# Performance work log

Hardware: AMD Instinct MI355X
Metric: run time of the kernel (lower is better)

Reference implementation:

```python
import jax, jax.numpy as jnp
import numpy as np

N_NODES = 100000


def gcn_conv(x, W, b, src, dst, n):
    """PyG GCNConv with default add_self_loops and symmetric normalization."""
    xw = x @ W  # [N, out]
    loop = jnp.arange(n, dtype=src.dtype)
    s = jnp.concatenate([src, loop])  # source j
    d = jnp.concatenate([dst, loop])  # target i
    deg = jax.ops.segment_sum(jnp.ones_like(d, dtype=xw.dtype), d, num_segments=n)
    dinv = jnp.where(deg > 0, jax.lax.rsqrt(deg), 0.0)
    norm = dinv[s] * dinv[d]  # [E+N]
    msg = xw[s] * norm[:, None]
    out = jax.ops.segment_sum(msg, d, num_segments=n)
    return out + b


def setup_inputs() -> dict:
    key = jax.random.key(0)
    ks = jax.random.split(key, 9)
    n, e, f = N_NODES, 1600000, 512
    x = jax.random.normal(ks[0], (n, f), dtype=jnp.float32)
    edge_index = jax.random.randint(ks[1], (2, e), 0, n, dtype=jnp.int32)
    y = jax.random.uniform(ks[2], (n, 1), dtype=jnp.float32)
    W1 = jax.random.normal(ks[3], (f, 64), dtype=jnp.float32) / np.sqrt(f)
    b1 = jnp.zeros((64,), jnp.float32)
    W2 = jax.random.normal(ks[4], (64, 256), dtype=jnp.float32) / np.sqrt(64)
    b2 = jnp.zeros((256,), jnp.float32)
    W3 = jax.random.normal(ks[5], (256, 1), dtype=jnp.float32) / np.sqrt(256)
    b3 = jnp.zeros((1,), jnp.float32)
    return {"x": x, "edge_index": edge_index, "y": y,
            "W1": W1, "b1": b1, "W2": W2, "b2": b2, "W3": W3, "b3": b3}


def reference(x, edge_index, y, W1, b1, W2, b2, W3, b3):
    n = x.shape[0]
    src, dst = edge_index[0], edge_index[1]
    h = jax.nn.relu(gcn_conv(x, W1, b1, src, dst, n))
    # dropout is identity in eval mode
    h = jax.nn.relu(gcn_conv(h, W2, b2, src, dst, n))
    z = gcn_conv(h, W3, b3, src, dst, n)  # logits [N, 1]
    # BCE(sigmoid(z), y), computed stably via log-sigmoid
    loss = -(y * jax.nn.log_sigmoid(z) + (1.0 - y) * jax.nn.log_sigmoid(-z))
    return jnp.mean(loss)
```

## Files before the change

### kernel.cpp

```cpp
#include <hip/hip_runtime.h>
#include <math.h>

typedef __attribute__((ext_vector_type(8))) short s16x8;
typedef __attribute__((ext_vector_type(4))) float f32x4;

__device__ inline ushort f2bf(float f) {
    union { float f; unsigned u; } v; v.f = f;
    unsigned r = v.u + 0x7FFF + ((v.u >> 16) & 1);
    return (ushort)(r >> 16);
}
__device__ inline float bf2f(ushort h) {
    union { unsigned u; float f; } v; v.u = ((unsigned)h) << 16;
    return v.f;
}
__device__ inline float bfLo(unsigned u) {
    union { unsigned x; float f; } v; v.x = u << 16; return v.f;
}
__device__ inline float bfHi(unsigned u) {
    union { unsigned x; float f; } v; v.x = u & 0xFFFF0000u; return v.f;
}


__global__ void hist_kernel(const int* __restrict__ dst, int E, int* __restrict__ cnt) {
    int e = blockIdx.x * blockDim.x + threadIdx.x;
    if (e < E) atomicAdd(&cnt[dst[e]], 1);
}

__global__ void alloc_kernel(const int* __restrict__ cnt, int* __restrict__ row_start,
                             float* __restrict__ dinv, int* __restrict__ total, int N) {
    int i = blockIdx.x * blockDim.x + threadIdx.x;
    int lane = threadIdx.x & 63;
    int c = (i < N) ? cnt[i] : 0;
    int inc = c;
#pragma unroll
    for (int o = 1; o < 64; o <<= 1) {
        int v = __shfl_up(inc, o, 64);
        if (lane >= o) inc += v;
    }
    int wsum = __shfl(inc, 63, 64);
    int base = 0;
    if (lane == 0) base = atomicAdd(total, wsum);
    base = __shfl(base, 0, 64);
    if (i < N) {
        row_start[i] = base + inc - c;
        dinv[i] = rsqrtf((float)(c + 1));
    }
}

__global__ void scatter_kernel(const int* __restrict__ src, const int* __restrict__ dst, int E,
                               const int* __restrict__ row_start, int* __restrict__ cursor,
                               int* __restrict__ csr) {
    int e = blockIdx.x * blockDim.x + threadIdx.x;
    if (e < E) {
        int d = dst[e];
        int p = row_start[d] + atomicAdd(&cursor[d], 1);
        csr[p] = src[e];
    }
}

__global__ void wsplit_kernel(const float* __restrict__ W, ushort* __restrict__ wt_hi,
                              ushort* __restrict__ wt_lo) {
    int idx = blockIdx.x * blockDim.x + threadIdx.x;
    if (idx < 64 * 512) {
        int n = idx & 63, k = idx >> 6;
        float f = W[k * 64 + n];
        ushort h = f2bf(f);
        wt_hi[n * 512 + k] = h;
        wt_lo[n * 512 + k] = f2bf(f - bf2f(h));
    }
}

__global__ __launch_bounds__(256, 3) void gemm1_kernel(const float* __restrict__ x,
                                                       const ushort* __restrict__ wt_hi,
                                                       const ushort* __restrict__ wt_lo,
                                                       const float* __restrict__ dinv,
                                                       ushort* __restrict__ out, int N) {
    __shared__ __align__(16) short xs_hi[128 * 64];
    __shared__ __align__(16) short xs_lo[128 * 64];
    __shared__ __align__(16) short ws_hi[64 * 64];
    __shared__ __align__(16) short ws_lo[64 * 64];

    const int tid = threadIdx.x;
    const int nodeBase = blockIdx.x * 128;
    const int wave = tid >> 6, lane = tid & 63;
    const int m16 = lane & 15, quad = lane >> 4;

    f32x4 acc[2][4];
#pragma unroll
    for (int mt = 0; mt < 2; mt++)
#pragma unroll
        for (int nt = 0; nt < 4; nt++) acc[mt][nt] = (f32x4){0.f, 0.f, 0.f, 0.f};

    for (int kc = 0; kc < 512; kc += 64) {
        __syncthreads();
#pragma unroll
        for (int i = 0; i < 4; i++) {
            int f = tid + i * 256;
            int node = f >> 3, g = f & 7;
            int gn = nodeBase + node;
            if (gn >= N) gn = N - 1;
            const float4 a = *(const float4*)(x + (size_t)gn * 512 + kc + g * 8);
            const float4 b = *(const float4*)(x + (size_t)gn * 512 + kc + g * 8 + 4);
            float ff[8] = {a.x, a.y, a.z, a.w, b.x, b.y, b.z, b.w};
            union { ushort u[8]; uint4 v; } H, L;
#pragma unroll
            for (int j = 0; j < 8; j++) {
                ushort h = f2bf(ff[j]);
                H.u[j] = h;
                L.u[j] = f2bf(ff[j] - bf2f(h));
            }
            int gp = (g + node) & 7;
            *(uint4*)&xs_hi[node * 64 + gp * 8] = H.v;
            *(uint4*)&xs_lo[node * 64 + gp * 8] = L.v;
        }
#pragma unroll
        for (int i = 0; i < 2; i++) {
            int f = tid + i * 256;
            int n = f >> 3, g = f & 7;
            int gp = (g + n) & 7;
            *(uint4*)&ws_hi[n * 64 + gp * 8] =
                *(const uint4*)(wt_hi + (size_t)n * 512 + kc + g * 8);
            *(uint4*)&ws_lo[n * 64 + gp * 8] =
                *(const uint4*)(wt_lo + (size_t)n * 512 + kc + g * 8);
        }
        __syncthreads();
#pragma unroll
        for (int ck = 0; ck < 2; ck++) {
            s16x8 Ah[2], Al[2];
#pragma unroll
            for (int mt = 0; mt < 2; mt++) {
                int row = (wave * 2 + mt) * 16 + m16;
                int gp = (ck * 4 + quad + row) & 7;
                Ah[mt] = *(s16x8*)&xs_hi[row * 64 + gp * 8];
                Al[mt] = *(s16x8*)&xs_lo[row * 64 + gp * 8];
            }
#pragma unroll
            for (int nt = 0; nt < 4; nt++) {
                int n = nt * 16 + m16;
                int gp = (ck * 4 + quad + n) & 7;
                s16x8 Bh = *(s16x8*)&ws_hi[n * 64 + gp * 8];
                s16x8 Bl = *(s16x8*)&ws_lo[n * 64 + gp * 8];
#pragma unroll
                for (int mt = 0; mt < 2; mt++) {
                    acc[mt][nt] = __builtin_amdgcn_mfma_f32_16x16x32_bf16(Ah[mt], Bh, acc[mt][nt], 0, 0, 0);
                    acc[mt][nt] = __builtin_amdgcn_mfma_f32_16x16x32_bf16(Ah[mt], Bl, acc[mt][nt], 0, 0, 0);
                    acc[mt][nt] = __builtin_amdgcn_mfma_f32_16x16x32_bf16(Al[mt], Bh, acc[mt][nt], 0, 0, 0);
                }
            }
        }
    }
#pragma unroll
    for (int mt = 0; mt < 2; mt++) {
#pragma unroll
        for (int r = 0; r < 4; r++) {
            int gn = nodeBase + (wave * 2 + mt) * 16 + quad * 4 + r;
            if (gn < N) {
                float di = dinv[gn];
#pragma unroll
                for (int nt = 0; nt < 4; nt++)
                    out[(size_t)gn * 64 + nt * 16 + m16] = f2bf(di * acc[mt][nt][r]);
            }
        }
    }
}

template <int RELU, int BIAS, int PREMUL>
__global__ void agg64bf_kernel(const ushort* __restrict__ in, ushort* __restrict__ out,
                               const int* __restrict__ row_start, const int* __restrict__ cnt,
                               const int* __restrict__ csr, const float* __restrict__ dinv,
                               const float* __restrict__ bias, int N) {
    int gw = (int)((blockIdx.x * (size_t)blockDim.x + threadIdx.x) >> 6);
    int lane = threadIdx.x & 63;
    if (gw >= N) return;
    float acc = bf2f(in[(size_t)gw * 64 + lane]);
    int s = row_start[gw];
    int c = cnt[gw];
    int e = 0;
    for (; e + 8 <= c; e += 8) {
        int j0 = csr[s + e + 0], j1 = csr[s + e + 1], j2 = csr[s + e + 2], j3 = csr[s + e + 3];
        int j4 = csr[s + e + 4], j5 = csr[s + e + 5], j6 = csr[s + e + 6], j7 = csr[s + e + 7];
        float v0 = bf2f(in[(size_t)j0 * 64 + lane]);
        float v1 = bf2f(in[(size_t)j1 * 64 + lane]);
        float v2 = bf2f(in[(size_t)j2 * 64 + lane]);
        float v3 = bf2f(in[(size_t)j3 * 64 + lane]);
        float v4 = bf2f(in[(size_t)j4 * 64 + lane]);
        float v5 = bf2f(in[(size_t)j5 * 64 + lane]);
        float v6 = bf2f(in[(size_t)j6 * 64 + lane]);
        float v7 = bf2f(in[(size_t)j7 * 64 + lane]);
        acc += ((v0 + v1) + (v2 + v3)) + ((v4 + v5) + (v6 + v7));
    }
    for (; e < c; e++) {
        int j = csr[s + e];
        acc += bf2f(in[(size_t)j * 64 + lane]);
    }
    float di = dinv[gw];
    float v = di * acc;
    if (BIAS) v += bias[lane];
    if (RELU) v = fmaxf(v, 0.f);
    if (PREMUL) v *= di;
    out[(size_t)gw * 64 + lane] = f2bf(v);
}

__global__ __launch_bounds__(256, 2) void gemm23_kernel(const ushort* __restrict__ a2,
                                                        const float* __restrict__ W2,
                                                        const float* __restrict__ b2,
                                                        const float* __restrict__ W3,
                                                        const float* __restrict__ dinv,
                                                        float* __restrict__ r, int N) {
    __shared__ float w2s[64 * 256];
    __shared__ float b2s[256];
    __shared__ float w3s[256];
    const int tid = threadIdx.x;
#pragma unroll
    for (int i = 0; i < 16; i++) {
        int f4 = tid + i * 256;
        *(float4*)&w2s[f4 * 4] = *(const float4*)&W2[f4 * 4];
    }
    b2s[tid] = b2[tid];
    w3s[tid] = W3[tid];
    __syncthreads();

    const int lane = tid & 63;
    const int wave = tid >> 6;
    const int nodeBase = blockIdx.x * 64 + wave * 16;

    float4 w3f = *(const float4*)&w3s[lane * 4];
    float4 b2f = *(const float4*)&b2s[lane * 4];

    float acc[16][4];
#pragma unroll
    for (int n = 0; n < 16; n++) {
        acc[n][0] = 0.f; acc[n][1] = 0.f; acc[n][2] = 0.f; acc[n][3] = 0.f;
    }

    for (int k4 = 0; k4 < 64; k4 += 4) {
        float4 wf0 = *(const float4*)&w2s[(k4 + 0) * 256 + lane * 4];
        float4 wf1 = *(const float4*)&w2s[(k4 + 1) * 256 + lane * 4];
        float4 wf2 = *(const float4*)&w2s[(k4 + 2) * 256 + lane * 4];
        float4 wf3 = *(const float4*)&w2s[(k4 + 3) * 256 + lane * 4];
#pragma unroll
        for (int n = 0; n < 16; n++) {
            int gn = nodeBase + n;
            if (gn >= N) gn = N - 1;
            uint2 u = *(const uint2*)(a2 + (size_t)gn * 64 + k4);
            float a0 = bfLo(u.x), a1 = bfHi(u.x), a2v = bfLo(u.y), a3 = bfHi(u.y);
            acc[n][0] = fmaf(a0, wf0.x, acc[n][0]);
            acc[n][1] = fmaf(a0, wf0.y, acc[n][1]);
            acc[n][2] = fmaf(a0, wf0.z, acc[n][2]);
            acc[n][3] = fmaf(a0, wf0.w, acc[n][3]);
            acc[n][0] = fmaf(a1, wf1.x, acc[n][0]);
            acc[n][1] = fmaf(a1, wf1.y, acc[n][1]);
            acc[n][2] = fmaf(a1, wf1.z, acc[n][2]);
            acc[n][3] = fmaf(a1, wf1.w, acc[n][3]);
            acc[n][0] = fmaf(a2v, wf2.x, acc[n][0]);
            acc[n][1] = fmaf(a2v, wf2.y, acc[n][1]);
            acc[n][2] = fmaf(a2v, wf2.z, acc[n][2]);
            acc[n][3] = fmaf(a2v, wf2.w, acc[n][3]);
            acc[n][0] = fmaf(a3, wf3.x, acc[n][0]);
            acc[n][1] = fmaf(a3, wf3.y, acc[n][1]);
            acc[n][2] = fmaf(a3, wf3.z, acc[n][2]);
            acc[n][3] = fmaf(a3, wf3.w, acc[n][3]);
        }
    }

#pragma unroll
    for (int n = 0; n < 16; n++) {
        float r0 = fmaxf(acc[n][0] + b2f.x, 0.f);
        float r1 = fmaxf(acc[n][1] + b2f.y, 0.f);
        float r2 = fmaxf(acc[n][2] + b2f.z, 0.f);
        float r3 = fmaxf(acc[n][3] + b2f.w, 0.f);
        float p = r0 * w3f.x + r1 * w3f.y + r2 * w3f.z + r3 * w3f.w;
#pragma unroll
        for (int off = 32; off > 0; off >>= 1) p += __shfl_down(p, off, 64);
        int gn = nodeBase + n;
        if (lane == 0 && gn < N) r[gn] = dinv[gn] * p;
    }
}

__global__ void loss_kernel(const float* __restrict__ r, const float* __restrict__ dinv,
                            const int* __restrict__ row_start, const int* __restrict__ cnt,
                            const int* __restrict__ csr, const float* __restrict__ y,
                            const float* __restrict__ b3, float* __restrict__ out,
                            int N, float invN) {
    int i = blockIdx.x * blockDim.x + threadIdx.x;
    float loss = 0.f;
    if (i < N) {
        float aedge = r[i];
        int s = row_start[i], c = cnt[i];
        int e = 0;
        for (; e + 4 <= c; e += 4) {
            int j0 = csr[s + e + 0], j1 = csr[s + e + 1];
            int j2 = csr[s + e + 2], j3 = csr[s + e + 3];
            aedge += (r[j0] + r[j1]) + (r[j2] + r[j3]);
        }
        for (; e < c; e++) aedge += r[csr[s + e]];
        float z = dinv[i] * aedge + b3[0];
        float yv = y[i];
        float L = log1pf(expf(-fabsf(z)));
        float spz  = fmaxf(z, 0.f) + L;
        float spnz = fmaxf(-z, 0.f) + L;
        loss = yv * spnz + (1.f - yv) * spz;
    }
#pragma unroll
    for (int off = 32; off > 0; off >>= 1) loss += __shfl_down(loss, off, 64);
    __shared__ float red[4];
    int lane = threadIdx.x & 63, wave = threadIdx.x >> 6;
    if (lane == 0) red[wave] = loss;
    __syncthreads();
    if (threadIdx.x == 0)
        atomicAdd(out, (red[0] + red[1] + red[2] + red[3]) * invN);
}

extern "C" void kernel_launch(void* const* d_in, const int* in_sizes, int n_in,
                              void* d_out, int out_size, void* d_ws, size_t ws_size,
                              hipStream_t stream) {
    const float* x  = (const float*)d_in[0];
    const int*   ei = (const int*)d_in[1];
    const float* y  = (const float*)d_in[2];
    const float* W1 = (const float*)d_in[3];
    const float* b1 = (const float*)d_in[4];
    const float* W2 = (const float*)d_in[5];
    const float* b2 = (const float*)d_in[6];
    const float* W3 = (const float*)d_in[7];
    const float* b3 = (const float*)d_in[8];

    const int N = in_sizes[2];
    const int E = in_sizes[1] / 2;
    const int* src  = ei;
    const int* dstp = ei + E;

    char* w = (char*)d_ws;
    int*    cnt       = (int*)w;    w += (size_t)N * 4;
    int*    cursor    = (int*)w;    w += (size_t)N * 4;
    int*    total     = (int*)w;    w += 16;
    int*    row_start = (int*)w;    w += (size_t)N * 4;
    float*  dinv      = (float*)w;  w += (size_t)N * 4;
    int*    csr       = (int*)w;    w += (size_t)E * 4;
    ushort* wt_hi     = (ushort*)w; w += (size_t)64 * 512 * 2;
    ushort* wt_lo     = (ushort*)w; w += (size_t)64 * 512 * 2;
    ushort* pbuf      = (ushort*)w; w += (size_t)N * 64 * 2;
    ushort* qbuf      = (ushort*)w; w += (size_t)N * 64 * 2;
    float*  rbuf      = (float*)w;  w += (size_t)N * 4;

    hipMemsetAsync(cnt, 0, (size_t)N * 8 + 16, stream);
    hipMemsetAsync(d_out, 0, sizeof(float), stream);

    const int tb = 256;
    wsplit_kernel<<<(64 * 512 + tb - 1) / tb, tb, 0, stream>>>(W1, wt_hi, wt_lo);
    hist_kernel<<<(E + tb - 1) / tb, tb, 0, stream>>>(dstp, E, cnt);
    alloc_kernel<<<(N + tb - 1) / tb, tb, 0, stream>>>(cnt, row_start, dinv, total, N);
    scatter_kernel<<<(E + tb - 1) / tb, tb, 0, stream>>>(src, dstp, E, row_start, cursor, csr);

    gemm1_kernel<<<(N + 127) / 128, 256, 0, stream>>>(x, wt_hi, wt_lo, dinv, pbuf, N);
    agg64bf_kernel<1, 1, 1><<<(N + 3) / 4, 256, 0, stream>>>(pbuf, qbuf, row_start, cnt, csr, dinv, b1, N);
    agg64bf_kernel<0, 0, 0><<<(N + 3) / 4, 256, 0, stream>>>(qbuf, pbuf, row_start, cnt, csr, dinv, nullptr, N);

    gemm23_kernel<<<(N + 63) / 64, 256, 0, stream>>>(pbuf, W2, b2, W3, dinv, rbuf, N);

    loss_kernel<<<(N + tb - 1) / tb, tb, 0, stream>>>(rbuf, dinv, row_start, cnt, csr, y, b3,
                                                      (float*)d_out, N, 1.0f / N);
}
```

Before: 722.1 us.

## Run layer-2 GEMM on MFMA with split-bf16 weights instead of FP32 FMAs

Replaces the scalar FP32 FMA loop in the fused layer-2/3 kernel with bf16 MFMA 16x16x32 instructions. W2 is pre-split into hi/lo bf16 halves by a new small kernel so the product keeps near-FP32 precision on the weight side. Each wave now covers 32 rows. The shared-memory staging of W2 is dropped, and weights are read straight from global memory and cache. The epilogue (bias, ReLU, dot with W3) is done per lane and reduced across 16 lanes with xor shuffles. The cost is an extra tiny launch and doubled MFMA work for the lo term.

After: 675.8 us. 1.07x faster.

```diff
diff --git a/kernel.cpp b/kernel.cpp
--- a/kernel.cpp
+++ b/kernel.cpp
@@ -67,6 +67,18 @@
         ushort h = f2bf(f);
         wt_hi[n * 512 + k] = h;
         wt_lo[n * 512 + k] = f2bf(f - bf2f(h));
+    }
+}
+
+__global__ void w2split_kernel(const float* __restrict__ W, ushort* __restrict__ wt_hi,
+                               ushort* __restrict__ wt_lo) {
+    int idx = blockIdx.x * blockDim.x + threadIdx.x;
+    if (idx < 64 * 256) {
+        int n = idx & 255, k = idx >> 8;
+        float f = W[k * 256 + n];
+        ushort h = f2bf(f);
+        wt_hi[n * 64 + k] = h;
+        wt_lo[n * 64 + k] = f2bf(f - bf2f(h));
     }
 }
 
@@ -202,78 +214,74 @@
 }
 
 __global__ __launch_bounds__(256, 2) void gemm23_kernel(const ushort* __restrict__ a2,
-                                                        const float* __restrict__ W2,
+                                                        const ushort* __restrict__ wt2_hi,
+                                                        const ushort* __restrict__ wt2_lo,
                                                         const float* __restrict__ b2,
                                                         const float* __restrict__ W3,
                                                         const float* __restrict__ dinv,
                                                         float* __restrict__ r, int N) {
-    __shared__ float w2s[64 * 256];
-    __shared__ float b2s[256];
-    __shared__ float w3s[256];
     const int tid = threadIdx.x;
-#pragma unroll
-    for (int i = 0; i < 16; i++) {
-        int f4 = tid + i * 256;
-        *(float4*)&w2s[f4 * 4] = *(const float4*)&W2[f4 * 4];
-    }
-    b2s[tid] = b2[tid];
-    w3s[tid] = W3[tid];
-    __syncthreads();
-
-    const int lane = tid & 63;
-    const int wave = tid >> 6;
-    const int nodeBase = blockIdx.x * 64 + wave * 16;
-
-    float4 w3f = *(const float4*)&w3s[lane * 4];
-    float4 b2f = *(const float4*)&b2s[lane * 4];
-
-    float acc[16][4];
-#pragma unroll
-    for (int n = 0; n < 16; n++) {
-        acc[n][0] = 0.f; acc[n][1] = 0.f; acc[n][2] = 0.f; acc[n][3] = 0.f;
-    }
-
-    for (int k4 = 0; k4 < 64; k4 += 4) {
-        float4 wf0 = *(const float4*)&w2s[(k4 + 0) * 256 + lane * 4];
-        float4 wf1 = *(const float4*)&w2s[(k4 + 1) * 256 + lane * 4];
-        float4 wf2 = *(const float4*)&w2s[(k4 + 2) * 256 + lane * 4];
-        float4 wf3 = *(const float4*)&w2s[(k4 + 3) * 256 + lane * 4];
-#pragma unroll
-        for (int n = 0; n < 16; n++) {
-            int gn = nodeBase + n;
-            if (gn >= N) gn = N - 1;
-            uint2 u = *(const uint2*)(a2 + (size_t)gn * 64 + k4);
-            float a0 = bfLo(u.x), a1 = bfHi(u.x), a2v = bfLo(u.y), a3 = bfHi(u.y);
-            acc[n][0] = fmaf(a0, wf0.x, acc[n][0]);
-            acc[n][1] = fmaf(a0, wf0.y, acc[n][1]);
-            acc[n][2] = fmaf(a0, wf0.z, acc[n][2]);
-            acc[n][3] = fmaf(a0, wf0.w, acc[n][3]);
-            acc[n][0] = fmaf(a1, wf1.x, acc[n][0]);
-            acc[n][1] = fmaf(a1, wf1.y, acc[n][1]);
-            acc[n][2] = fmaf(a1, wf1.z, acc[n][2]);
-            acc[n][3] = fmaf(a1, wf1.w, acc[n][3]);
-            acc[n][0] = fmaf(a2v, wf2.x, acc[n][0]);
-            acc[n][1] = fmaf(a2v, wf2.y, acc[n][1]);
-            acc[n][2] = fmaf(a2v, wf2.z, acc[n][2]);
-            acc[n][3] = fmaf(a2v, wf2.w, acc[n][3]);
-            acc[n][0] = fmaf(a3, wf3.x, acc[n][0]);
-            acc[n][1] = fmaf(a3, wf3.y, acc[n][1]);
-            acc[n][2] = fmaf(a3, wf3.z, acc[n][2]);
-            acc[n][3] = fmaf(a3, wf3.w, acc[n][3]);
-        }
-    }
-
-#pragma unroll
-    for (int n = 0; n < 16; n++) {
-        float r0 = fmaxf(acc[n][0] + b2f.x, 0.f);
-        float r1 = fmaxf(acc[n][1] + b2f.y, 0.f);
-        float r2 = fmaxf(acc[n][2] + b2f.z, 0.f);
-        float r3 = fmaxf(acc[n][3] + b2f.w, 0.f);
-        float p = r0 * w3f.x + r1 * w3f.y + r2 * w3f.z + r3 * w3f.w;
-#pragma unroll
-        for (int off = 32; off > 0; off >>= 1) p += __shfl_down(p, off, 64);
-        int gn = nodeBase + n;
-        if (lane == 0 && gn < N) r[gn] = dinv[gn] * p;
+    const int wave = tid >> 6, lane = tid & 63;
+    const int m16 = lane & 15, quad = lane >> 4;
+    const int rowBase = blockIdx.x * 128 + wave * 32;
+
+    s16x8 A[2][2];
+#pragma unroll
+    for (int mt = 0; mt < 2; mt++) {
+        int gn = rowBase + mt * 16 + m16;
+        if (gn >= N) gn = N - 1;
+        const ushort* ap = a2 + (size_t)gn * 64 + quad * 8;
+#pragma unroll
+        for (int ck = 0; ck < 2; ck++)
+            A[mt][ck] = *(const s16x8*)(ap + ck * 32);
+    }
+
+    f32x4 acc[2][16];
+#pragma unroll
+    for (int mt = 0; mt < 2; mt++)
+#pragma unroll
+        for (int nt = 0; nt < 16; nt++) acc[mt][nt] = (f32x4){0.f, 0.f, 0.f, 0.f};
+
+#pragma unroll
+    for (int nt = 0; nt < 16; nt++) {
+        int n = nt * 16 + m16;
+        const ushort* bh = wt2_hi + (size_t)n * 64 + quad * 8;
+        const ushort* bl = wt2_lo + (size_t)n * 64 + quad * 8;
+        s16x8 Bh0 = *(const s16x8*)(bh);
+        s16x8 Bh1 = *(const s16x8*)(bh + 32);
+        s16x8 Bl0 = *(const s16x8*)(bl);
+        s16x8 Bl1 = *(const s16x8*)(bl + 32);
+        acc[0][nt] = __builtin_amdgcn_mfma_f32_16x16x32_bf16(A[0][0], Bh0, acc[0][nt], 0, 0, 0);
+        acc[1][nt] = __builtin_amdgcn_mfma_f32_16x16x32_bf16(A[1][0], Bh0, acc[1][nt], 0, 0, 0);
+        acc[0][nt] = __builtin_amdgcn_mfma_f32_16x16x32_bf16(A[0][1], Bh1, acc[0][nt], 0, 0, 0);
+        acc[1][nt] = __builtin_amdgcn_mfma_f32_16x16x32_bf16(A[1][1], Bh1, acc[1][nt], 0, 0, 0);
+        acc[0][nt] = __builtin_amdgcn_mfma_f32_16x16x32_bf16(A[0][0], Bl0, acc[0][nt], 0, 0, 0);
+        acc[1][nt] = __builtin_amdgcn_mfma_f32_16x16x32_bf16(A[1][0], Bl0, acc[1][nt], 0, 0, 0);
+        acc[0][nt] = __builtin_amdgcn_mfma_f32_16x16x32_bf16(A[0][1], Bl1, acc[0][nt], 0, 0, 0);
+        acc[1][nt] = __builtin_amdgcn_mfma_f32_16x16x32_bf16(A[1][1], Bl1, acc[1][nt], 0, 0, 0);
+    }
+
+    float bv[16], wv[16];
+#pragma unroll
+    for (int nt = 0; nt < 16; nt++) {
+        bv[nt] = b2[nt * 16 + m16];
+        wv[nt] = W3[nt * 16 + m16];
+    }
+#pragma unroll
+    for (int mt = 0; mt < 2; mt++) {
+#pragma unroll
+        for (int rr = 0; rr < 4; rr++) {
+            float p = 0.f;
+#pragma unroll
+            for (int nt = 0; nt < 16; nt++) {
+                float v = fmaxf(acc[mt][nt][rr] + bv[nt], 0.f);
+                p = fmaf(v, wv[nt], p);
+            }
+#pragma unroll
+            for (int off = 1; off < 16; off <<= 1) p += __shfl_xor(p, off, 64);
+            int gn = rowBase + mt * 16 + quad * 4 + rr;
+            if (m16 == 0 && gn < N) r[gn] = dinv[gn] * p;
+        }
     }
 }
 
@@ -338,6 +346,8 @@
     int*    csr       = (int*)w;    w += (size_t)E * 4;
     ushort* wt_hi     = (ushort*)w; w += (size_t)64 * 512 * 2;
     ushort* wt_lo     = (ushort*)w; w += (size_t)64 * 512 * 2;
+    ushort* wt2_hi    = (ushort*)w; w += (size_t)256 * 64 * 2;
+    ushort* wt2_lo    = (ushort*)w; w += (size_t)256 * 64 * 2;
     ushort* pbuf      = (ushort*)w; w += (size_t)N * 64 * 2;
     ushort* qbuf      = (ushort*)w; w += (size_t)N * 64 * 2;
     float*  rbuf      = (float*)w;  w += (size_t)N * 4;
@@ -347,6 +357,7 @@
 
     const int tb = 256;
     wsplit_kernel<<<(64 * 512 + tb - 1) / tb, tb, 0, stream>>>(W1, wt_hi, wt_lo);
+    w2split_kernel<<<(64 * 256 + tb - 1) / tb, tb, 0, stream>>>(W2, wt2_hi, wt2_lo);
     hist_kernel<<<(E + tb - 1) / tb, tb, 0, stream>>>(dstp, E, cnt);
     alloc_kernel<<<(N + tb - 1) / tb, tb, 0, stream>>>(cnt, row_start, dinv, total, N);
     scatter_kernel<<<(E + tb - 1) / tb, tb, 0, stream>>>(src, dstp, E, row_start, cursor, csr);
@@ -355,7 +366,7 @@
     agg64bf_kernel<1, 1, 1><<<(N + 3) / 4, 256, 0, stream>>>(pbuf, qbuf, row_start, cnt, csr, dinv, b1, N);
     agg64bf_kernel<0, 0, 0><<<(N + 3) / 4, 256, 0, stream>>>(qbuf, pbuf, row_start, cnt, csr, dinv, nullptr, N);
 
-    gemm23_kernel<<<(N + 63) / 64, 256, 0, stream>>>(pbuf, W2, b2, W3, dinv, rbuf, N);
+    gemm23_kernel<<<(N + 127) / 128, 256, 0, stream>>>(pbuf, wt2_hi, wt2_lo, b2, W3, dinv, rbuf, N);
 
     loss_kernel<<<(N + tb - 1) / tb, tb, 0, stream>>>(rbuf, dinv, row_start, cnt, csr, y, b3,
                                                       (float*)d_out, N, 1.0f / N);
```
